# Optimization experiments

Measured on AMD Instinct MI355X. Metric: run time of the kernel, lower is better.

The kernel has to match this reference:

```python
import jax, jax.numpy as jnp
import numpy as np

B, T, H, IN, OUT, FUT = 256, 512, 512, 1, 1, 16


def setup_inputs() -> dict:
    key = jax.random.key(0)
    ks = jax.random.split(key, 11)
    bound = 1.0 / np.sqrt(H)  # torch LSTMCell/Linear default init
    u = lambda kk, sh: jax.random.uniform(kk, sh, jnp.float32, -bound, bound)
    fbias = lambda b: b.at[H:2 * H].set(1.0)  # forget-gate bias filled with 1.0 per __init__
    return {
        "x": jax.random.normal(ks[0], (B, T), jnp.float32),
        "Wih0": u(ks[1], (4 * H, IN)),
        "Whh0": u(ks[2], (4 * H, H)),
        "bih0": fbias(u(ks[3], (4 * H,))),
        "bhh0": fbias(u(ks[4], (4 * H,))),
        "Wih1": u(ks[5], (4 * H, H)),
        "Whh1": u(ks[6], (4 * H, H)),
        "bih1": fbias(u(ks[7], (4 * H,))),
        "bhh1": fbias(u(ks[8], (4 * H,))),
        "Wlin": u(ks[9], (OUT, H)),
        "blin": u(ks[10], (OUT,)),
        "future": FUT,
    }


def _cell(xv, h, c, Wih, Whh, bih, bhh):
    # torch.nn.LSTMCell: gates ordered (i, f, g, o)
    gates = xv @ Wih.T + h @ Whh.T + bih + bhh
    i, f, g, o = jnp.split(gates, 4, axis=-1)
    c = jax.nn.sigmoid(f) * c + jax.nn.sigmoid(i) * jnp.tanh(g)
    h = jax.nn.sigmoid(o) * jnp.tanh(c)
    return h, c


def reference(x, Wih0, Whh0, bih0, bhh0, Wih1, Whh1, bih1, bhh1, Wlin, blin, future):
    params = ((Wih0, Whh0, bih0, bhh0), (Wih1, Whh1, bih1, bhh1))
    Bsz, hid = x.shape[0], Whh0.shape[1]
    h0 = tuple(jnp.zeros((Bsz, hid), x.dtype) for _ in params)
    c0 = tuple(jnp.zeros((Bsz, hid), x.dtype) for _ in params)

    def layer_stack(inp, hs, cs):
        new_h, new_c = [], []
        for j, (Wih, Whh, bih, bhh) in enumerate(params):
            h, c = _cell(inp, hs[j], cs[j], Wih, Whh, bih, bhh)
            new_h.append(h)
            new_c.append(c)
            inp = h
        return tuple(new_h), tuple(new_c), inp

    def cond_step(carry, xt):  # xt: [B, 1]
        hs, cs = carry
        hs, cs, top = layer_stack(xt, hs, cs)
        out = top @ Wlin.T + blin  # [B, 1]
        return (hs, cs), out

    xs = jnp.swapaxes(x, 0, 1)[:, :, None]  # [T, B, 1]
    (hs, cs), outs = jax.lax.scan(cond_step, (h0, c0), xs)
    last = outs[-1]

    def fut_step(carry, _):
        hs, cs, out = carry
        hs, cs, top = layer_stack(out, hs, cs)
        out = top @ Wlin.T + blin
        return (hs, cs, out), out

    _, fut_outs = jax.lax.scan(fut_step, (hs, cs, last), None, length=future)

    all_outs = jnp.concatenate([outs, fut_outs], axis=0)  # [T+future, B, 1]
    return jnp.swapaxes(all_outs, 0, 1)[:, :, 0]  # [B, T+future]
```

## Files before the change

### kernel.cpp

```cpp
#include <hip/hip_runtime.h>
#include <hip/hip_bf16.h>
#include <math.h>

#define HID    512
#define BATCH  256
#define TLEN   512
#define FUT    16
#define NSTEP  (TLEN + FUT)
#define NGRP   16
#define WPG    16
#define BPG    16
#define UPW    32
#define NR     128

#define OFF_W0   0u
#define OFF_W1   2097152u
#define OFF_CA   6291456u
#define OFF_XF   7340032u
#define OFF_WI   7357440u
#define OFF_B0   7365632u
#define OFF_B1   7373824u
#define OFF_BAR  7382016u
#define OFF_XT   7384064u

typedef __bf16 bf16x8 __attribute__((ext_vector_type(8)));
typedef float  f32x4  __attribute__((ext_vector_type(4)));

__device__ __forceinline__ float sigf(float v)      { return 1.f / (1.f + __expf(-v)); }
__device__ __forceinline__ float tanh_fast(float v) { return 2.f / (1.f + __expf(-2.f * v)) - 1.f; }

__device__ __forceinline__ void store_short_llc(void* p, unsigned short v) {
    asm volatile("global_store_short %0, %1, off sc0 sc1"
                 :: "v"(p), "v"((unsigned)v) : "memory");
}

__device__ __forceinline__ void gl2lds16_llc(const void* g, void* l) {
    __builtin_amdgcn_global_load_lds(
        (const __attribute__((address_space(1))) void*)g,
        (__attribute__((address_space(3))) void*)l, 16, 0, 17);
}

__device__ __forceinline__ void flag_barrier(unsigned* flags, int m, unsigned phase) {
    __builtin_amdgcn_s_waitcnt(0);
    __syncthreads();
    if (threadIdx.x == 0)
        __hip_atomic_store(&flags[m], phase, __ATOMIC_RELAXED, __HIP_MEMORY_SCOPE_AGENT);
    if (threadIdx.x < 64) {
        const int lane = threadIdx.x;
        const bool active = (lane < WPG) && (lane != m);
        for (;;) {
            unsigned f = phase;
            if (active)
                f = __hip_atomic_load(&flags[lane], __ATOMIC_RELAXED, __HIP_MEMORY_SCOPE_AGENT);
            if (__ballot(f >= phase) == ~0ull) break;
            __builtin_amdgcn_s_sleep(1);
        }
    }
    __syncthreads();
}

__global__ void lstm_init(char* __restrict__ ws, float* __restrict__ out,
                          const float* __restrict__ blin)
{
    float bl = blin[0];
    int tid = blockIdx.x * blockDim.x + threadIdx.x;
    int stride = gridDim.x * blockDim.x;
    uint4* ca = (uint4*)(ws + OFF_CA);
    for (int i = tid; i < 65536; i += stride) ca[i] = make_uint4(0u, 0u, 0u, 0u);
    float* xf = (float*)(ws + OFF_XF);
    for (int i = tid; i < (FUT + 1) * BATCH; i += stride) xf[i] = bl;
    unsigned* bar = (unsigned*)(ws + OFF_BAR);
    for (int i = tid; i < NGRP * 32; i += stride) bar[i] = 0u;
    for (int i = tid; i < BATCH * NSTEP; i += stride) out[i] = bl;
}

__global__ void lstm_pack(char* __restrict__ ws,
    const float* __restrict__ x,
    const float* __restrict__ Wih0, const float* __restrict__ Whh0,
    const float* __restrict__ bih0, const float* __restrict__ bhh0,
    const float* __restrict__ Wih1, const float* __restrict__ Whh1,
    const float* __restrict__ bih1, const float* __restrict__ bhh1)
{
    int tid = blockIdx.x * blockDim.x + threadIdx.x;
    int stride = gridDim.x * blockDim.x;

    __hip_bfloat16* W0p = (__hip_bfloat16*)(ws + OFF_W0);
    for (int i = tid; i < 16 * 128 * 512; i += stride) {
        int k = i & 511, r = (i >> 9) & 127, m = i >> 16;
        int row = (r >> 5) * HID + m * UPW + (r & 31);
        W0p[i] = __float2bfloat16(Whh0[(size_t)row * HID + k]);
    }
    __hip_bfloat16* W1p = (__hip_bfloat16*)(ws + OFF_W1);
    for (int i = tid; i < 16 * 128 * 1024; i += stride) {
        int k = i & 1023, r = (i >> 10) & 127, m = i >> 17;
        int row = (r >> 5) * HID + m * UPW + (r & 31);
        float v = (k < 512) ? Wih1[(size_t)row * HID + k] : Whh1[(size_t)row * HID + (k - 512)];
        W1p[i] = __float2bfloat16(v);
    }
    float* wi = (float*)(ws + OFF_WI);
    float* b0 = (float*)(ws + OFF_B0);
    float* b1 = (float*)(ws + OFF_B1);
    for (int i = tid; i < 16 * 128; i += stride) {
        int r = i & 127, m = i >> 7;
        int row = (r >> 5) * HID + m * UPW + (r & 31);
        wi[i] = Wih0[row];
        b0[i] = bih0[row] + bhh0[row];
        b1[i] = bih1[row] + bhh1[row];
    }
    float* xT = (float*)(ws + OFF_XT);
    for (int i = tid; i < TLEN * BATCH; i += stride) {
        int t = i >> 8, b = i & 255;
        xT[i] = x[(size_t)b * TLEN + t];
    }
}

__global__ __launch_bounds__(512, 2) void lstm_persist(
    const float* __restrict__ wlin,
    float* __restrict__ out, char* __restrict__ ws)
{
    const int tid  = threadIdx.x;
    const int lane = tid & 63;
    const int wave = tid >> 6;
    const int g    = blockIdx.x & 15;
    const int m    = blockIdx.x >> 4;
    const int bbase = g * BPG;

    __shared__ __attribute__((aligned(16))) __hip_bfloat16 As[16 * 1024];
    __shared__ float g0S[16][136];
    __shared__ float g1S[16][136];
    char* AsB = (char*)As;

    {
        int* az = (int*)As;
        for (int i = tid; i < (16 * 1024 * 2) / 4; i += 512) az[i] = 0;
    }

    const float* wis = (const float*)(ws + OFF_WI) + m * NR;
    const float* b0s = (const float*)(ws + OFF_B0) + m * NR;
    const float* b1s = (const float*)(ws + OFF_B1) + m * NR;
    char* CAg = ws + OFF_CA + (size_t)g * 65536;
    float* xfeed = (float*)(ws + OFF_XF);
    const float* xT = (const float*)(ws + OFF_XT);
    unsigned* flags = (unsigned*)(ws + OFF_BAR) + g * 32;

    const int fl = lane & 15;
    const int fq = lane >> 4;
    const int w  = wave;
    const int us  = tid & 31;
    const int b0r = tid >> 5;

    const float wl0 = wlin[m * UPW + us];
    float wiR[4], b0R[4], b1R[4];
#pragma unroll
    for (int q = 0; q < 4; ++q) {
        wiR[q] = wis[q * 32 + us];
        b0R[q] = b0s[q * 32 + us];
        b1R[q] = b1s[q * 32 + us];
    }
    float c00 = 0.f, c10 = 0.f;

    const int cgr  = 4 * m + (us >> 3);
    const int pub0 = b0r * 1024 + (((cgr + b0r) & 63) << 4) + (us & 7) * 2;

    const bf16x8* W0row = (const bf16x8*)(ws + OFF_W0 + (size_t)m * NR * 512 * 2)
                          + (size_t)(w * 16 + fl) * 64;
    const bf16x8* W1row = (const bf16x8*)(ws + OFF_W1 + (size_t)m * NR * 1024 * 2)
                          + (size_t)(w * 16 + fl) * 128;
    bf16x8 w0f[16], w1f[32];
#pragma unroll
    for (int ks = 0; ks < 16; ++ks) w0f[ks] = W0row[ks * 4 + fq];
#pragma unroll
    for (int ks = 0; ks < 32; ++ks) w1f[ks] = W1row[ks * 4 + fq];

    __syncthreads();

    const bf16x8* Asv = (const bf16x8*)As;

    unsigned phase = 0;
    for (int t = 0; t < NSTEP; ++t) {
        const int p = t & 1;
        char* CAp = CAg + p * 32768;
        char* CAq = CAg + (1 - p) * 32768;

        float xv0;
        if (t < TLEN) {
            xv0 = xT[t * BATCH + bbase + b0r];
        } else {
            xv0 = xfeed[(t - TLEN) * BATCH + bbase + b0r];
        }

        f32x4 acc0 = {0.f, 0.f, 0.f, 0.f};
#pragma unroll
        for (int ks = 0; ks < 16; ++ks) {
            int c = ks * 4 + fq;
            bf16x8 a0 = Asv[fl * 128 + ((c + fl) & 63)];
            acc0 = __builtin_amdgcn_mfma_f32_16x16x32_bf16(a0, w0f[ks], acc0, 0, 0, 0);
        }
#pragma unroll
        for (int i = 0; i < 4; ++i)
            g0S[fq * 4 + i][w * 16 + fl] = acc0[i];
        __syncthreads();

        {
            float gi = g0S[b0r][us]      + b0R[0] + xv0 * wiR[0];
            float gf = g0S[b0r][32 + us] + b0R[1] + xv0 * wiR[1];
            float gg = g0S[b0r][64 + us] + b0R[2] + xv0 * wiR[2];
            float go = g0S[b0r][96 + us] + b0R[3] + xv0 * wiR[3];
            c00 = sigf(gf) * c00 + sigf(gi) * tanh_fast(gg);
            __hip_bfloat16 h = __float2bfloat16(sigf(go) * tanh_fast(c00));
            store_short_llc(CAp + pub0, *(unsigned short*)&h);
        }

        ++phase;
        flag_barrier(flags, m, phase);

        {
#pragma unroll
            for (int ci = 0; ci < 2; ++ci) {
                int b = wave * 2 + ci;
                gl2lds16_llc(CAp + b * 1024 + lane * 16,
                             AsB + b * 2048 + lane * 16);
                gl2lds16_llc(CAq + 16384 + b * 1024 + lane * 16,
                             AsB + b * 2048 + 1024 + lane * 16);
            }
            __builtin_amdgcn_s_waitcnt(0);
            __syncthreads();
        }

        acc0 = (f32x4){0.f, 0.f, 0.f, 0.f};
#pragma unroll
        for (int ks = 0; ks < 16; ++ks) {
            int c = ks * 4 + fq;
            bf16x8 a0 = Asv[fl * 128 + ((c + fl) & 63)];
            acc0 = __builtin_amdgcn_mfma_f32_16x16x32_bf16(a0, w1f[ks], acc0, 0, 0, 0);
        }
#pragma unroll
        for (int ks = 16; ks < 32; ++ks) {
            int c = (ks - 16) * 4 + fq;
            bf16x8 a0 = Asv[fl * 128 + 64 + ((c + fl) & 63)];
            acc0 = __builtin_amdgcn_mfma_f32_16x16x32_bf16(a0, w1f[ks], acc0, 0, 0, 0);
        }
#pragma unroll
        for (int i = 0; i < 4; ++i)
            g1S[fq * 4 + i][w * 16 + fl] = acc0[i];
        __syncthreads();

        {
            float gi = g1S[b0r][us]      + b1R[0];
            float gf = g1S[b0r][32 + us] + b1R[1];
            float gg = g1S[b0r][64 + us] + b1R[2];
            float go = g1S[b0r][96 + us] + b1R[3];
            c10 = sigf(gf) * c10 + sigf(gi) * tanh_fast(gg);
            float h = sigf(go) * tanh_fast(c10);
            __hip_bfloat16 hb = __float2bfloat16(h);
            store_short_llc(CAp + 16384 + pub0, *(unsigned short*)&hb);
            float po = wl0 * h;
#pragma unroll
            for (int off = 1; off < 32; off <<= 1) po += __shfl_xor(po, off, 64);
            if (us == 0) {
                atomicAdd(&out[(size_t)(bbase + b0r) * NSTEP + t], po);
                if (t >= TLEN - 1)
                    atomicAdd(&xfeed[(t - (TLEN - 1)) * BATCH + bbase + b0r], po);
            }
        }

        if (t >= TLEN - 1) {
            ++phase;
            flag_barrier(flags, m, phase);
        }
    }
}

extern "C" void kernel_launch(void* const* d_in, const int* in_sizes, int n_in,
                              void* d_out, int out_size, void* d_ws, size_t ws_size,
                              hipStream_t stream)
{
    const float* x    = (const float*)d_in[0];
    const float* Wih0 = (const float*)d_in[1];
    const float* Whh0 = (const float*)d_in[2];
    const float* bih0 = (const float*)d_in[3];
    const float* bhh0 = (const float*)d_in[4];
    const float* Wih1 = (const float*)d_in[5];
    const float* Whh1 = (const float*)d_in[6];
    const float* bih1 = (const float*)d_in[7];
    const float* bhh1 = (const float*)d_in[8];
    const float* Wlin = (const float*)d_in[9];
    const float* blin = (const float*)d_in[10];
    float* out = (float*)d_out;
    char* ws = (char*)d_ws;

    hipLaunchKernelGGL(lstm_init, dim3(256), dim3(256), 0, stream, ws, out, blin);
    hipLaunchKernelGGL(lstm_pack, dim3(512), dim3(256), 0, stream,
                       ws, x, Wih0, Whh0, bih0, bhh0, Wih1, Whh1, bih1, bhh1);
    hipLaunchKernelGGL(lstm_persist, dim3(256), dim3(512), 0, stream, Wlin, out, ws);
}
```

Baseline: 2.359 ms.

## Replace group flag barrier with per-producer flag waits and chunked exchange layout

Each block now publishes its h chunks (layer 0 and layer 1) as one contiguous per-block region, and each wave waits only on the flags of the two producer blocks whose chunks it copies into LDS, instead of a full group barrier followed by copying. The LDS A-operand indexing changes from a swizzled layout to the plain chunked one. The intent is to overlap waiting with copying and avoid a full all-to-all barrier on every step. It drops the bank-conflict swizzle and relies on relaxed flag ordering after s_waitcnt for visibility, which could be fragile.

```diff
diff --git a/kernel.cpp b/kernel.cpp
--- a/kernel.cpp
+++ b/kernel.cpp
@@ -159,8 +159,7 @@
     }
     float c00 = 0.f, c10 = 0.f;
 
-    const int cgr  = 4 * m + (us >> 3);
-    const int pub0 = b0r * 1024 + (((cgr + b0r) & 63) << 4) + (us & 7) * 2;
+    const int pubm = m * 2048 + b0r * 64 + us * 2;
 
     const bf16x8* W0row = (const bf16x8*)(ws + OFF_W0 + (size_t)m * NR * 512 * 2)
                           + (size_t)(w * 16 + fl) * 64;
@@ -192,8 +191,7 @@
         f32x4 acc0 = {0.f, 0.f, 0.f, 0.f};
 #pragma unroll
         for (int ks = 0; ks < 16; ++ks) {
-            int c = ks * 4 + fq;
-            bf16x8 a0 = Asv[fl * 128 + ((c + fl) & 63)];
+            bf16x8 a0 = Asv[ks * 128 + fl * 4 + fq];
             acc0 = __builtin_amdgcn_mfma_f32_16x16x32_bf16(a0, w0f[ks], acc0, 0, 0, 0);
         }
 #pragma unroll
@@ -208,36 +206,39 @@
             float go = g0S[b0r][96 + us] + b0R[3] + xv0 * wiR[3];
             c00 = sigf(gf) * c00 + sigf(gi) * tanh_fast(gg);
             __hip_bfloat16 h = __float2bfloat16(sigf(go) * tanh_fast(c00));
-            store_short_llc(CAp + pub0, *(unsigned short*)&h);
-        }
-
+            store_short_llc(CAp + pubm, *(unsigned short*)&h);
+        }
+
+        __builtin_amdgcn_s_waitcnt(0);
+        __syncthreads();
         ++phase;
-        flag_barrier(flags, m, phase);
-
-        {
-#pragma unroll
-            for (int ci = 0; ci < 2; ++ci) {
-                int b = wave * 2 + ci;
-                gl2lds16_llc(CAp + b * 1024 + lane * 16,
-                             AsB + b * 2048 + lane * 16);
-                gl2lds16_llc(CAq + 16384 + b * 1024 + lane * 16,
-                             AsB + b * 2048 + 1024 + lane * 16);
+        if (tid == 0)
+            __hip_atomic_store(&flags[m], phase, __ATOMIC_RELAXED, __HIP_MEMORY_SCOPE_AGENT);
+#pragma unroll
+        for (int jj = 0; jj < 2; ++jj) {
+            int j = wave * 2 + jj;
+            if (j != m) {
+                while (__hip_atomic_load(&flags[j], __ATOMIC_RELAXED,
+                                         __HIP_MEMORY_SCOPE_AGENT) < phase)
+                    __builtin_amdgcn_s_sleep(1);
             }
-            __builtin_amdgcn_s_waitcnt(0);
-            __syncthreads();
-        }
+            gl2lds16_llc(CAp + j * 2048 + lane * 16,
+                         AsB + j * 2048 + lane * 16);
+            gl2lds16_llc(CAq + j * 2048 + 1024 + lane * 16,
+                         AsB + j * 2048 + 1024 + lane * 16);
+        }
+        __builtin_amdgcn_s_waitcnt(0);
+        __syncthreads();
 
         acc0 = (f32x4){0.f, 0.f, 0.f, 0.f};
 #pragma unroll
         for (int ks = 0; ks < 16; ++ks) {
-            int c = ks * 4 + fq;
-            bf16x8 a0 = Asv[fl * 128 + ((c + fl) & 63)];
+            bf16x8 a0 = Asv[ks * 128 + fl * 4 + fq];
             acc0 = __builtin_amdgcn_mfma_f32_16x16x32_bf16(a0, w1f[ks], acc0, 0, 0, 0);
         }
 #pragma unroll
         for (int ks = 16; ks < 32; ++ks) {
-            int c = (ks - 16) * 4 + fq;
-            bf16x8 a0 = Asv[fl * 128 + 64 + ((c + fl) & 63)];
+            bf16x8 a0 = Asv[(ks - 16) * 128 + 64 + fl * 4 + fq];
             acc0 = __builtin_amdgcn_mfma_f32_16x16x32_bf16(a0, w1f[ks], acc0, 0, 0, 0);
         }
 #pragma unroll
@@ -253,7 +254,7 @@
             c10 = sigf(gf) * c10 + sigf(gi) * tanh_fast(gg);
             float h = sigf(go) * tanh_fast(c10);
             __hip_bfloat16 hb = __float2bfloat16(h);
-            store_short_llc(CAp + 16384 + pub0, *(unsigned short*)&hb);
+            store_short_llc(CAp + pubm + 1024, *(unsigned short*)&hb);
             float po = wl0 * h;
 #pragma unroll
             for (int off = 1; off < 32; off <<= 1) po += __shfl_xor(po, off, 64);
```

Result: slower. 2.535 ms (+7.5%).
